# Optimization experiments

Measured on AMD Instinct MI355X. Metric: run time of the kernel, lower is better.

The kernel has to match this reference:

```python
import jax, jax.numpy as jnp
import numpy as np

N_NODES = 20000
N_RELS = 64
RP = 8
EMB = 64
N_CLASSES = 16
NT = 250000      # unique (subject, object) pairs
N_TRIPLES = 500000


def setup_inputs() -> dict:
    rng = np.random.default_rng(0)
    # sample candidate (s, o) pairs, dedupe (mirrors torch.unique(pairs, dim=0)),
    # keep exactly NT unique pairs
    cand = rng.integers(0, N_NODES, size=(NT + 60000, 2))
    pairs = np.unique(cand, axis=0)
    assert pairs.shape[0] >= NT
    pairs = pairs[:NT]
    # each triple maps to a unique-pair row and a relation column;
    # relation_matrix is the coalesced sparse_coo (nt, num_rels) densified
    row = rng.integers(0, NT, size=N_TRIPLES)
    rel = rng.integers(0, N_RELS, size=N_TRIPLES)
    relation_matrix = np.zeros((NT, N_RELS), dtype=np.float32)
    np.add.at(relation_matrix, (row, rel), 1.0)
    # hindices / vindices exactly as in __init__ (note the literal o*r / s*r):
    s, o = pairs[:, 0].astype(np.int64), pairs[:, 1].astype(np.int64)
    rm = np.arange(RP, dtype=np.int64)[:, None]
    hrow = np.tile(s, RP)                      # (RP*NT,) row in [0, N)
    hcol = (o[None, :] * rm).reshape(-1)       # (RP*NT,) col in [0, N*RP)
    vrow = (s[None, :] * rm).reshape(-1)       # (RP*NT,) row in [0, N*RP)
    vcol = np.tile(o, RP)                      # (RP*NT,) col in [0, N)

    key = jax.random.key(0)
    ks = jax.random.split(key, 6)

    def xavier(k, shape, fan_in, fan_out):
        gain = np.float32(np.sqrt(2.0))  # calculate_gain('relu')
        bound = gain * np.float32(np.sqrt(6.0 / (fan_in + fan_out)))
        return jax.random.uniform(k, shape, jnp.float32, -bound, bound)

    lb = np.float32(1.0 / np.sqrt(N_RELS))  # nn.Linear default init bound
    return {
        "relation_matrix": jnp.asarray(relation_matrix),
        "hrow": jnp.asarray(hrow), "hcol": jnp.asarray(hcol),
        "vrow": jnp.asarray(vrow), "vcol": jnp.asarray(vcol),
        "W_l1": jax.random.uniform(ks[0], (N_RELS, RP), jnp.float32, -lb, lb),
        "b_l1": jax.random.uniform(ks[1], (RP,), jnp.float32, -lb, lb),
        "W_l2": jax.random.uniform(ks[2], (N_RELS, RP), jnp.float32, -lb, lb),
        "b_l2": jax.random.uniform(ks[3], (RP,), jnp.float32, -lb, lb),
        "weights1": xavier(ks[4], (RP, N_NODES, EMB), N_NODES * EMB, RP * EMB),
        "weights2": xavier(ks[5], (RP, EMB, N_CLASSES), EMB * N_CLASSES, RP * N_CLASSES),
        "bias1": jnp.zeros((EMB,), jnp.float32),
        "bias2": jnp.zeros((N_CLASSES,), jnp.float32),
    }


def reference(relation_matrix, hrow, hcol, vrow, vcol,
              W_l1, b_l1, W_l2, b_l2, weights1, weights2, bias1, bias2):
    n, rp, e = N_NODES, RP, EMB
    nrp = n * rp
    # ---- hop 1: latent coefficients (to_latent1, ldepth=0 => single Linear)
    l1 = relation_matrix @ W_l1 + b_l1              # (NT, RP)
    l1 = l1.T.reshape(-1)                           # (RP*NT,) r-major, matches h/v index order
    # sum_sparse(hindices, l1, (n, n*rp), row=False): per-edge column-sum normalization
    colsum = jax.ops.segment_sum(l1, hcol, num_segments=nrp)
    l1 = l1 / colsum[hcol]
    # spmm over hindices: out[hrow] += l1 * weights1.view(n*rp, e)[hcol]
    Wflat = weights1.reshape(nrp, e)                # (N*RP, EMB)
    h = jax.ops.segment_sum(l1[:, None] * Wflat[hcol], hrow, num_segments=n)
    h = jax.nn.relu(h + bias1)                      # (N, EMB)
    # ---- hop 2
    l2 = jax.nn.softmax(relation_matrix @ W_l2 + b_l2, axis=1)  # (NT, RP)
    l2 = jax.nn.relu(l2.T.reshape(-1))              # (RP*NT,)
    # sum_sparse(vindices, l2, (n*rp, n), row=True): per-edge row-sum normalization
    rowsum = jax.ops.segment_sum(l2, vrow, num_segments=nrp)
    l2 = l2 / jnp.maximum(rowsum[vrow], 1e-6)
    # spmm over vindices: out[vrow] += l2 * h[vcol]
    h2 = jax.ops.segment_sum(l2[:, None] * h[vcol], vrow, num_segments=nrp)
    h2 = h2.reshape(rp, n, e)                       # (RP, N, EMB)
    logits = jnp.einsum('rhc,rnh->nc', weights2, h2) + bias2  # (N, C)
    return logits
```

## Files before the change

kernel.cpp:

```cpp
#include <hip/hip_runtime.h>
#include <hip/hip_fp16.h>

#define NT      250000
#define NN      20000
#define RP      8
#define EMB     64
#define NCLS    16
#define NRELS   64
#define COLB    547
#define REDB    64
#define KMAX    140000
#define RPB     79
#define HIB     977
#define MISCB   1250

__global__ __launch_bounds__(256) void k_gemv(
    const float* __restrict__ rm,
    const float* __restrict__ W1, const float* __restrict__ b1,
    const float* __restrict__ W2, const float* __restrict__ b2,
    float* __restrict__ l1, float* __restrict__ l2)
{
    __shared__ float tile[256 * 20];
    int t = threadIdx.x;
    int base = blockIdx.x * 256;
    float a1[8], a2[8];
#pragma unroll
    for (int r = 0; r < 8; ++r) { a1[r] = b1[r]; a2[r] = b2[r]; }

#pragma unroll 1
    for (int kc = 0; kc < 4; ++kc) {
        __syncthreads();
#pragma unroll
        for (int q = 0; q < 4; ++q) {
            int i = q * 256 + t;
            int pl = i >> 2, j4 = i & 3;
            int p = base + pl;
            float4 v = make_float4(0.f, 0.f, 0.f, 0.f);
            if (p < NT) v = reinterpret_cast<const float4*>(rm)[(size_t)p * 16 + kc * 4 + j4];
            *reinterpret_cast<float4*>(&tile[pl * 20 + j4 * 4]) = v;
        }
        __syncthreads();
        float xr[16];
#pragma unroll
        for (int j4 = 0; j4 < 4; ++j4) {
            float4 v = *reinterpret_cast<const float4*>(&tile[t * 20 + j4 * 4]);
            xr[j4 * 4 + 0] = v.x; xr[j4 * 4 + 1] = v.y;
            xr[j4 * 4 + 2] = v.z; xr[j4 * 4 + 3] = v.w;
        }
#pragma unroll
        for (int kk = 0; kk < 16; ++kk) {
            float x = xr[kk];
            int k = kc * 16 + kk;
#pragma unroll
            for (int r = 0; r < 8; ++r) {
                a1[r] = fmaf(x, W1[k * 8 + r], a1[r]);
                a2[r] = fmaf(x, W2[k * 8 + r], a2[r]);
            }
        }
    }
    int p = base + t;
    if (p >= NT) return;
    float mx = a2[0];
#pragma unroll
    for (int r = 1; r < 8; ++r) mx = fmaxf(mx, a2[r]);
    float sm = 0.f;
#pragma unroll
    for (int r = 0; r < 8; ++r) { a2[r] = __expf(a2[r] - mx); sm += a2[r]; }
    float inv = 1.0f / sm;
#pragma unroll
    for (int r = 0; r < 8; ++r) a2[r] *= inv;
    float4* o1 = reinterpret_cast<float4*>(l1 + (size_t)p * 8);
    float4* o2 = reinterpret_cast<float4*>(l2 + (size_t)p * 8);
    o1[0] = make_float4(a1[0], a1[1], a1[2], a1[3]);
    o1[1] = make_float4(a1[4], a1[5], a1[6], a1[7]);
    o2[0] = make_float4(a2[0], a2[1], a2[2], a2[3]);
    o2[1] = make_float4(a2[4], a2[5], a2[6], a2[7]);
}

__global__ __launch_bounds__(256) void k_init(
    const int* __restrict__ hrow, int* __restrict__ rowptr,
    const int* __restrict__ vcol, int* __restrict__ cnt)
{
    int bid = blockIdx.x;
    if (bid < RPB) {
        int i = bid * 256 + threadIdx.x;
        if (i > NN) return;
        int lo = 0, hi = NT;
        while (lo < hi) { int mid = (lo + hi) >> 1; if (hrow[mid] < i) lo = mid + 1; else hi = mid; }
        rowptr[i] = lo;
    } else {
        int p = (bid - RPB) * 256 + threadIdx.x;
        if (p < NT) atomicAdd(&cnt[vcol[p]], 1);
    }
}

__global__ __launch_bounds__(1024) void k_scan(
    const int* __restrict__ cnt, int* __restrict__ cstart, int* __restrict__ cnt2)
{
    __shared__ int part[1024];
    int t = threadIdx.x;
    int base = t * 20;
    int local[20];
    int s = 0;
#pragma unroll
    for (int i = 0; i < 20; ++i) {
        int idx = base + i;
        int c = (idx < NN) ? cnt[idx] : 0;
        local[i] = s;
        s += c;
    }
    part[t] = s;
    __syncthreads();
    for (int off = 1; off < 1024; off <<= 1) {
        int v = (t >= off) ? part[t - off] : 0;
        __syncthreads();
        part[t] += v;
        __syncthreads();
    }
    int ebase = t ? part[t - 1] : 0;
#pragma unroll
    for (int i = 0; i < 20; ++i) {
        int idx = base + i;
        if (idx < NN) { cstart[idx] = ebase + local[i]; cnt2[idx] = ebase + local[i]; }
    }
    if (t == 1023) cstart[NN] = part[1023];
}

__global__ __launch_bounds__(256) void k_pos(
    const int* __restrict__ vcol, int* __restrict__ cnt2, int* __restrict__ cscidx)
{
    int p = blockIdx.x * blockDim.x + threadIdx.x;
    if (p >= NT) return;
    int o = vcol[p];
    int slot = atomicAdd(&cnt2[o], 1);
    cscidx[slot] = p;
}

__global__ __launch_bounds__(256) void k_colsum(
    const float* __restrict__ l1, const int* __restrict__ cstart,
    const int* __restrict__ cscidx, float* __restrict__ colsum)
{
    int bid = blockIdx.x;
    if (bid < COLB) {
        int tid = bid * 256 + threadIdx.x;
        if (tid < NN * 7) {
            int o = tid / 7;
            int r = tid - o * 7 + 1;
            int qb = cstart[o], qe = cstart[o + 1];
            float s = 0.f;
            for (int q = qb; q < qe; ++q)
                s += l1[(size_t)cscidx[q] * 8 + r];
            atomicAdd(&colsum[o * r], s);
        }
    } else {
        int b2 = bid - COLB;
        float s = 0.f;
        for (int i = b2 * 256 + threadIdx.x; i < NT; i += REDB * 256) s += l1[(size_t)i * 8];
        __shared__ float red[256];
        red[threadIdx.x] = s;
        __syncthreads();
        for (int off = 128; off > 0; off >>= 1) {
            if (threadIdx.x < off) red[threadIdx.x] += red[threadIdx.x + off];
            __syncthreads();
        }
        if (threadIdx.x == 0) atomicAdd(&colsum[0], red[0]);
    }
}

__global__ __launch_bounds__(256) void k_inv(float* __restrict__ cs)
{
    int i = blockIdx.x * blockDim.x + threadIdx.x;
    if (i < RP * NN) cs[i] = 1.0f / cs[i];
}

__global__ __launch_bounds__(256) void k_contrib(
    const float* __restrict__ l1, const float* __restrict__ ics,
    const int* __restrict__ cstart, const int* __restrict__ cscidx,
    const float* __restrict__ w1, __half* __restrict__ contrib)
{
    int o = (int)((blockIdx.x * blockDim.x + threadIdx.x) >> 6);
    int lane = threadIdx.x & 63;
    if (o >= NN) return;
    int qb = cstart[o], qe = cstart[o + 1];
    if (qb == qe) return;
    float y[8];
    y[0] = w1[lane] * ics[0];
#pragma unroll
    for (int r = 1; r < 8; ++r) {
        int seg = o * r;
        y[r] = w1[(size_t)seg * EMB + lane] * ics[seg];
    }
    int q = qb;
    for (; q + 1 < qe; q += 2) {
        int p0 = cscidx[q], p1 = cscidx[q + 1];
        const float4* a4 = reinterpret_cast<const float4*>(l1 + (size_t)p0 * 8);
        const float4* b4 = reinterpret_cast<const float4*>(l1 + (size_t)p1 * 8);
        float4 A = a4[0], B = a4[1], C = b4[0], D = b4[1];
        float v0 = A.x * y[0];
        v0 = fmaf(A.y, y[1], v0); v0 = fmaf(A.z, y[2], v0); v0 = fmaf(A.w, y[3], v0);
        v0 = fmaf(B.x, y[4], v0); v0 = fmaf(B.y, y[5], v0);
        v0 = fmaf(B.z, y[6], v0); v0 = fmaf(B.w, y[7], v0);
        float v1 = C.x * y[0];
        v1 = fmaf(C.y, y[1], v1); v1 = fmaf(C.z, y[2], v1); v1 = fmaf(C.w, y[3], v1);
        v1 = fmaf(D.x, y[4], v1); v1 = fmaf(D.y, y[5], v1);
        v1 = fmaf(D.z, y[6], v1); v1 = fmaf(D.w, y[7], v1);
        contrib[(size_t)p0 * EMB + lane] = __float2half(v0);
        contrib[(size_t)p1 * EMB + lane] = __float2half(v1);
    }
    if (q < qe) {
        int p0 = cscidx[q];
        const float4* a4 = reinterpret_cast<const float4*>(l1 + (size_t)p0 * 8);
        float4 A = a4[0], B = a4[1];
        float v0 = A.x * y[0];
        v0 = fmaf(A.y, y[1], v0); v0 = fmaf(A.z, y[2], v0); v0 = fmaf(A.w, y[3], v0);
        v0 = fmaf(B.x, y[4], v0); v0 = fmaf(B.y, y[5], v0);
        v0 = fmaf(B.z, y[6], v0); v0 = fmaf(B.w, y[7], v0);
        contrib[(size_t)p0 * EMB + lane] = __float2half(v0);
    }
}

__global__ __launch_bounds__(256) void k_h(
    const __half* __restrict__ contrib, const float* __restrict__ l2,
    const int* __restrict__ rowptr, const float* __restrict__ bias1,
    __half* __restrict__ h, float* __restrict__ rowsum, float* __restrict__ rs0part)
{
    int s = (int)((blockIdx.x * blockDim.x + threadIdx.x) >> 6);
    int lane = threadIdx.x & 63;
    if (s >= NN) return;
    int pb = rowptr[s], pe = rowptr[s + 1];
    float acc = 0.f;
    for (int p = pb; p < pe; ++p)
        acc += __half2float(contrib[(size_t)p * EMB + lane]);
    h[(size_t)s * EMB + lane] = __float2half(fmaxf(acc + bias1[lane], 0.f));

    float psum = 0.f;
    for (int p0 = pb + (lane >> 3); p0 < pe; p0 += 8)
        psum += l2[(size_t)p0 * 8 + (lane & 7)];
    psum += __shfl_xor(psum, 8, 64);
    psum += __shfl_xor(psum, 16, 64);
    psum += __shfl_xor(psum, 32, 64);
    if (s == 0) {
        float tt = psum;
        tt += __shfl_xor(tt, 1, 64);
        tt += __shfl_xor(tt, 2, 64);
        tt += __shfl_xor(tt, 4, 64);
        if (lane == 0) rs0part[0] = tt;
    } else {
        if (lane == 0) rs0part[s] = psum;
        else if (lane < 8) atomicAdd(&rowsum[s * lane], psum);
    }
}

__global__ __launch_bounds__(256) void k_misc(
    float* __restrict__ rs, float* __restrict__ out, const float* __restrict__ b2,
    const float* __restrict__ rs0part)
{
    int bid = blockIdx.x;
    if (bid < MISCB) {
        int i = bid * 256 + threadIdx.x;
        if (i >= 1 && i < KMAX) rs[i] = 1.0f / fmaxf(rs[i], 1e-6f);
        if (i < NN * NCLS) out[i] = b2[i & (NCLS - 1)];
    } else {
        __shared__ float red[256];
        float sv = 0.f;
        for (int i = threadIdx.x; i < NN; i += 256) sv += rs0part[i];
        red[threadIdx.x] = sv;
        __syncthreads();
        for (int off = 128; off > 0; off >>= 1) {
            if (threadIdx.x < off) red[threadIdx.x] += red[threadIdx.x + off];
            __syncthreads();
        }
        if (threadIdx.x == 0) rs[0] = 1.0f / fmaxf(red[0], 1e-6f);
    }
}

__global__ __launch_bounds__(256) void k_l2out(
    const float* __restrict__ l2, const int* __restrict__ rowptr,
    const int* __restrict__ vcol, const __half* __restrict__ h,
    const float* __restrict__ irs, const float* __restrict__ w2,
    float* __restrict__ out, float* __restrict__ Abuf0)
{
    int s = (int)((blockIdx.x * blockDim.x + threadIdx.x) >> 6);
    int lane = threadIdx.x & 63;
    if (s >= NN) return;
    int pb = rowptr[s], pe = rowptr[s + 1];
    float sc[8];
#pragma unroll
    for (int rr = 1; rr < 8; ++rr) sc[rr] = (s > 0) ? irs[s * rr] : 0.f;
    float acc[8];
#pragma unroll
    for (int r = 0; r < 8; ++r) acc[r] = 0.f;
    int p = pb;
    for (; p + 3 < pe; p += 4) {
        int o0 = vcol[p], o1 = vcol[p + 1], o2 = vcol[p + 2], o3 = vcol[p + 3];
        float hv0 = __half2float(h[(size_t)o0 * EMB + lane]);
        float hv1 = __half2float(h[(size_t)o1 * EMB + lane]);
        float hv2 = __half2float(h[(size_t)o2 * EMB + lane]);
        float hv3 = __half2float(h[(size_t)o3 * EMB + lane]);
        const float4* q4 = reinterpret_cast<const float4*>(l2 + (size_t)p * 8);
        float4 A = q4[0], B = q4[1], C = q4[2], D = q4[3];
        float4 E = q4[4], F = q4[5], G = q4[6], H = q4[7];
        acc[0] = fmaf(A.x, hv0, fmaf(C.x, hv1, fmaf(E.x, hv2, fmaf(G.x, hv3, acc[0]))));
        acc[1] = fmaf(A.y, hv0, fmaf(C.y, hv1, fmaf(E.y, hv2, fmaf(G.y, hv3, acc[1]))));
        acc[2] = fmaf(A.z, hv0, fmaf(C.z, hv1, fmaf(E.z, hv2, fmaf(G.z, hv3, acc[2]))));
        acc[3] = fmaf(A.w, hv0, fmaf(C.w, hv1, fmaf(E.w, hv2, fmaf(G.w, hv3, acc[3]))));
        acc[4] = fmaf(B.x, hv0, fmaf(D.x, hv1, fmaf(F.x, hv2, fmaf(H.x, hv3, acc[4]))));
        acc[5] = fmaf(B.y, hv0, fmaf(D.y, hv1, fmaf(F.y, hv2, fmaf(H.y, hv3, acc[5]))));
        acc[6] = fmaf(B.z, hv0, fmaf(D.z, hv1, fmaf(F.z, hv2, fmaf(H.z, hv3, acc[6]))));
        acc[7] = fmaf(B.w, hv0, fmaf(D.w, hv1, fmaf(F.w, hv2, fmaf(H.w, hv3, acc[7]))));
    }
    for (; p < pe; ++p) {
        int o0 = vcol[p];
        float hv0 = __half2float(h[(size_t)o0 * EMB + lane]);
        const float4* q4 = reinterpret_cast<const float4*>(l2 + (size_t)p * 8);
        float4 A = q4[0], B = q4[1];
        acc[0] = fmaf(A.x, hv0, acc[0]); acc[1] = fmaf(A.y, hv0, acc[1]);
        acc[2] = fmaf(A.z, hv0, acc[2]); acc[3] = fmaf(A.w, hv0, acc[3]);
        acc[4] = fmaf(B.x, hv0, acc[4]); acc[5] = fmaf(B.y, hv0, acc[5]);
        acc[6] = fmaf(B.z, hv0, acc[6]); acc[7] = fmaf(B.w, hv0, acc[7]);
    }
    if (s == 0) {
        float a = acc[0] + acc[1] + acc[2] + acc[3] +
                  acc[4] + acc[5] + acc[6] + acc[7];
        Abuf0[lane] = a;
        return;
    }
    Abuf0[(size_t)s * EMB + lane] = acc[0];
    if (pb == pe) return;
    int hq = lane >> 4, c = lane & 15;
#pragma unroll
    for (int rr = 1; rr < 8; ++rr) {
        int k = s * rr;
        int rp = k / NN;
        int n  = k - rp * NN;
        float v = 0.f;
#pragma unroll
        for (int hh = 0; hh < 16; ++hh) {
            float av = __shfl(acc[rr], hq * 16 + hh, 64);
            v = fmaf(av, w2[((rp * EMB) + (hq * 16 + hh)) * NCLS + c], v);
        }
        v += __shfl_xor(v, 16, 64);
        v += __shfl_xor(v, 32, 64);
        if (lane < 16) atomicAdd(&out[(size_t)n * NCLS + lane], v * sc[rr]);
    }
}

__global__ __launch_bounds__(256) void k_redA(
    const float* __restrict__ Abuf0, float* __restrict__ h0row)
{
    __shared__ float red[256];
    int lane = threadIdx.x & 63, w = threadIdx.x >> 6;
    float sum = 0.f;
    for (int ss = blockIdx.x + 64 * w; ss < NN; ss += 256)
        sum += Abuf0[(size_t)ss * EMB + lane];
    red[threadIdx.x] = sum;
    __syncthreads();
    if (threadIdx.x < 64) {
        float v = red[threadIdx.x] + red[threadIdx.x + 64] +
                  red[threadIdx.x + 128] + red[threadIdx.x + 192];
        atomicAdd(&h0row[threadIdx.x], v);
    }
}

__global__ __launch_bounds__(64) void k_out0(
    const float* __restrict__ h0row, const float* __restrict__ irs0,
    const float* __restrict__ w2, float* __restrict__ out)
{
    int hq = threadIdx.x >> 4, c = threadIdx.x & 15;
    float v = 0.f;
#pragma unroll
    for (int hh = 0; hh < 16; ++hh) {
        int hd = hq * 16 + hh;
        v = fmaf(h0row[hd], w2[hd * NCLS + c], v);
    }
    v += __shfl_xor(v, 16, 64);
    v += __shfl_xor(v, 32, 64);
    if (threadIdx.x < 16) atomicAdd(&out[c], v * irs0[0]);
}

extern "C" void kernel_launch(void* const* d_in, const int* in_sizes, int n_in,
                              void* d_out, int out_size, void* d_ws, size_t ws_size,
                              hipStream_t stream)
{
    const float* rm    = (const float*)d_in[0];
    const int*   hrow  = (const int*)d_in[1];
    const int*   vcol  = (const int*)d_in[4];
    const float* W1    = (const float*)d_in[5];
    const float* b1    = (const float*)d_in[6];
    const float* W2    = (const float*)d_in[7];
    const float* b2    = (const float*)d_in[8];
    const float* w1    = (const float*)d_in[9];
    const float* w2    = (const float*)d_in[10];
    const float* bias1 = (const float*)d_in[11];
    const float* bias2 = (const float*)d_in[12];
    float* out = (float*)d_out;

    float* ws = (float*)d_ws;
    float*  l1      = ws;
    float*  l2      = ws + 2000000;
    int*    rowptr  = (int*)(ws + 4000000);
    float*  h0row   = ws + 4030000;
    float*  colsum  = ws + 4100000;
    float*  rowsum  = ws + 4260000;
    __half* h       = (__half*)(ws + 4400000);
    int*    cnt     = (int*)(ws + 5040000);
    int*    cstart  = cnt + 20000;
    int*    cnt2    = cstart + 20001;
    int*    cscidx  = cnt2 + 20000;
    __half* contrib = (__half*)(ws + 5600000);
    float*  Abuf0   = ws;
    float*  rs0part = ws + 1280000;

    hipMemsetAsync(colsum, 0, (size_t)160000 * sizeof(float), stream);
    hipMemsetAsync(rowsum, 0, (size_t)KMAX * sizeof(float), stream);
    hipMemsetAsync(h0row, 0, (size_t)64 * sizeof(float), stream);
    hipMemsetAsync(cnt, 0, (size_t)20000 * sizeof(int), stream);

    k_init   <<<RPB + HIB, 256, 0, stream>>>(hrow, rowptr, vcol, cnt);
    k_scan   <<<1, 1024, 0, stream>>>(cnt, cstart, cnt2);
    k_pos    <<<(NT + 255) / 256, 256, 0, stream>>>(vcol, cnt2, cscidx);
    k_gemv   <<<(NT + 255) / 256, 256, 0, stream>>>(rm, W1, b1, W2, b2, l1, l2);
    k_colsum <<<COLB + REDB, 256, 0, stream>>>(l1, cstart, cscidx, colsum);
    k_inv    <<<(RP * NN + 255) / 256, 256, 0, stream>>>(colsum);
    k_contrib<<<(NN * 64) / 256, 256, 0, stream>>>(l1, colsum, cstart, cscidx, w1, contrib);
    k_h      <<<(NN * 64) / 256, 256, 0, stream>>>(contrib, l2, rowptr, bias1, h, rowsum, rs0part);
    k_misc   <<<MISCB + 1, 256, 0, stream>>>(rowsum, out, bias2, rs0part);
    k_l2out  <<<(NN * 64) / 256, 256, 0, stream>>>(l2, rowptr, vcol, h, rowsum, w2, out, Abuf0);
    k_redA   <<<64, 256, 0, stream>>>(Abuf0, h0row);
    k_out0   <<<1, 64, 0, stream>>>(h0row, rowsum, w2, out);
}
```

Measured before the change: 251.3 us.

## Fuse init into gemv, parallelize colsum per wave, drop inverse and out0 kernels

The rowptr binary search and the vcol histogram become extra blocks of the gemv kernel, and the separate inverse kernel is removed by dividing by colsum directly in k_contrib. The out0 projection is folded into k_redA: each block projects its partial sum through w2 and atomically adds to out, so the h0row buffer and its memset go away. k_colsum is restructured to use one wavefront per column, with lanes split across 8 entries times 8 relations and a shuffle reduction, replacing the serial per-thread loop with uncoalesced reads. The aim is fewer launches and better memory parallelism; the cost is more atomics into out (one per block instead of one in total) and a divide in place of a multiply in k_contrib.

```diff
diff --git a/kernel.cpp b/kernel.cpp
--- a/kernel.cpp
+++ b/kernel.cpp
@@ -7,9 +7,9 @@
 #define EMB     64
 #define NCLS    16
 #define NRELS   64
-#define COLB    547
 #define REDB    64
 #define KMAX    140000
+#define GEMVB   977
 #define RPB     79
 #define HIB     977
 #define MISCB   1250
@@ -18,11 +18,28 @@
     const float* __restrict__ rm,
     const float* __restrict__ W1, const float* __restrict__ b1,
     const float* __restrict__ W2, const float* __restrict__ b2,
-    float* __restrict__ l1, float* __restrict__ l2)
+    float* __restrict__ l1, float* __restrict__ l2,
+    const int* __restrict__ hrow, int* __restrict__ rowptr,
+    const int* __restrict__ vcol, int* __restrict__ cnt)
 {
     __shared__ float tile[256 * 20];
+    int bid = blockIdx.x;
+    if (bid >= GEMVB) {
+        int b = bid - GEMVB;
+        if (b < RPB) {
+            int i = b * 256 + threadIdx.x;
+            if (i > NN) return;
+            int lo = 0, hi = NT;
+            while (lo < hi) { int mid = (lo + hi) >> 1; if (hrow[mid] < i) lo = mid + 1; else hi = mid; }
+            rowptr[i] = lo;
+        } else {
+            int p = (b - RPB) * 256 + threadIdx.x;
+            if (p < NT) atomicAdd(&cnt[vcol[p]], 1);
+        }
+        return;
+    }
     int t = threadIdx.x;
-    int base = blockIdx.x * 256;
+    int base = bid * 256;
     float a1[8], a2[8];
 #pragma unroll
     for (int r = 0; r < 8; ++r) { a1[r] = b1[r]; a2[r] = b2[r]; }
@@ -77,23 +94,6 @@
     o2[1] = make_float4(a2[4], a2[5], a2[6], a2[7]);
 }
 
-__global__ __launch_bounds__(256) void k_init(
-    const int* __restrict__ hrow, int* __restrict__ rowptr,
-    const int* __restrict__ vcol, int* __restrict__ cnt)
-{
-    int bid = blockIdx.x;
-    if (bid < RPB) {
-        int i = bid * 256 + threadIdx.x;
-        if (i > NN) return;
-        int lo = 0, hi = NT;
-        while (lo < hi) { int mid = (lo + hi) >> 1; if (hrow[mid] < i) lo = mid + 1; else hi = mid; }
-        rowptr[i] = lo;
-    } else {
-        int p = (bid - RPB) * 256 + threadIdx.x;
-        if (p < NT) atomicAdd(&cnt[vcol[p]], 1);
-    }
-}
-
 __global__ __launch_bounds__(1024) void k_scan(
     const int* __restrict__ cnt, int* __restrict__ cstart, int* __restrict__ cnt2)
 {
@@ -141,19 +141,23 @@
     const int* __restrict__ cscidx, float* __restrict__ colsum)
 {
     int bid = blockIdx.x;
-    if (bid < COLB) {
-        int tid = bid * 256 + threadIdx.x;
-        if (tid < NN * 7) {
-            int o = tid / 7;
-            int r = tid - o * 7 + 1;
-            int qb = cstart[o], qe = cstart[o + 1];
-            float s = 0.f;
-            for (int q = qb; q < qe; ++q)
-                s += l1[(size_t)cscidx[q] * 8 + r];
-            atomicAdd(&colsum[o * r], s);
-        }
+    if (bid < NN / 4) {
+        int o = bid * 4 + (threadIdx.x >> 6);
+        int lane = threadIdx.x & 63;
+        int qb = cstart[o], qe = cstart[o + 1];
+        if (qb == qe) return;
+        int j = lane >> 3, r = lane & 7;
+        float sum = 0.f;
+        for (int q0 = qb; q0 < qe; q0 += 8) {
+            int q = q0 + j;
+            if (q < qe) sum += l1[(size_t)cscidx[q] * 8 + r];
+        }
+        sum += __shfl_xor(sum, 8, 64);
+        sum += __shfl_xor(sum, 16, 64);
+        sum += __shfl_xor(sum, 32, 64);
+        if (lane >= 1 && lane < 8) atomicAdd(&colsum[o * lane], sum);
     } else {
-        int b2 = bid - COLB;
+        int b2 = bid - NN / 4;
         float s = 0.f;
         for (int i = b2 * 256 + threadIdx.x; i < NT; i += REDB * 256) s += l1[(size_t)i * 8];
         __shared__ float red[256];
@@ -167,14 +171,8 @@
     }
 }
 
-__global__ __launch_bounds__(256) void k_inv(float* __restrict__ cs)
-{
-    int i = blockIdx.x * blockDim.x + threadIdx.x;
-    if (i < RP * NN) cs[i] = 1.0f / cs[i];
-}
-
 __global__ __launch_bounds__(256) void k_contrib(
-    const float* __restrict__ l1, const float* __restrict__ ics,
+    const float* __restrict__ l1, const float* __restrict__ colsum,
     const int* __restrict__ cstart, const int* __restrict__ cscidx,
     const float* __restrict__ w1, __half* __restrict__ contrib)
 {
@@ -184,11 +182,11 @@
     int qb = cstart[o], qe = cstart[o + 1];
     if (qb == qe) return;
     float y[8];
-    y[0] = w1[lane] * ics[0];
+    y[0] = w1[lane] / colsum[0];
 #pragma unroll
     for (int r = 1; r < 8; ++r) {
         int seg = o * r;
-        y[r] = w1[(size_t)seg * EMB + lane] * ics[seg];
+        y[r] = w1[(size_t)seg * EMB + lane] / colsum[seg];
     }
     int q = qb;
     for (; q + 1 < qe; q += 2) {
@@ -346,9 +344,11 @@
 }
 
 __global__ __launch_bounds__(256) void k_redA(
-    const float* __restrict__ Abuf0, float* __restrict__ h0row)
+    const float* __restrict__ Abuf0, const float* __restrict__ irs,
+    const float* __restrict__ w2, float* __restrict__ out)
 {
     __shared__ float red[256];
+    __shared__ float part[64];
     int lane = threadIdx.x & 63, w = threadIdx.x >> 6;
     float sum = 0.f;
     for (int ss = blockIdx.x + 64 * w; ss < NN; ss += 256)
@@ -356,26 +356,22 @@
     red[threadIdx.x] = sum;
     __syncthreads();
     if (threadIdx.x < 64) {
-        float v = red[threadIdx.x] + red[threadIdx.x + 64] +
-                  red[threadIdx.x + 128] + red[threadIdx.x + 192];
-        atomicAdd(&h0row[threadIdx.x], v);
-    }
-}
-
-__global__ __launch_bounds__(64) void k_out0(
-    const float* __restrict__ h0row, const float* __restrict__ irs0,
-    const float* __restrict__ w2, float* __restrict__ out)
-{
-    int hq = threadIdx.x >> 4, c = threadIdx.x & 15;
-    float v = 0.f;
-#pragma unroll
-    for (int hh = 0; hh < 16; ++hh) {
-        int hd = hq * 16 + hh;
-        v = fmaf(h0row[hd], w2[hd * NCLS + c], v);
-    }
-    v += __shfl_xor(v, 16, 64);
-    v += __shfl_xor(v, 32, 64);
-    if (threadIdx.x < 16) atomicAdd(&out[c], v * irs0[0]);
+        part[threadIdx.x] = red[threadIdx.x] + red[threadIdx.x + 64] +
+                            red[threadIdx.x + 128] + red[threadIdx.x + 192];
+    }
+    __syncthreads();
+    if (threadIdx.x < 64) {
+        int hq = threadIdx.x >> 4, c = threadIdx.x & 15;
+        float v = 0.f;
+#pragma unroll
+        for (int hh = 0; hh < 16; ++hh) {
+            int hd = hq * 16 + hh;
+            v = fmaf(part[hd], w2[hd * NCLS + c], v);
+        }
+        v += __shfl_xor(v, 16, 64);
+        v += __shfl_xor(v, 32, 64);
+        if (threadIdx.x < 16) atomicAdd(&out[c], v * irs[0]);
+    }
 }
 
 extern "C" void kernel_launch(void* const* d_in, const int* in_sizes, int n_in,
@@ -399,7 +395,6 @@
     float*  l1      = ws;
     float*  l2      = ws + 2000000;
     int*    rowptr  = (int*)(ws + 4000000);
-    float*  h0row   = ws + 4030000;
     float*  colsum  = ws + 4100000;
     float*  rowsum  = ws + 4260000;
     __half* h       = (__half*)(ws + 4400000);
@@ -413,19 +408,16 @@
 
     hipMemsetAsync(colsum, 0, (size_t)160000 * sizeof(float), stream);
     hipMemsetAsync(rowsum, 0, (size_t)KMAX * sizeof(float), stream);
-    hipMemsetAsync(h0row, 0, (size_t)64 * sizeof(float), stream);
     hipMemsetAsync(cnt, 0, (size_t)20000 * sizeof(int), stream);
 
-    k_init   <<<RPB + HIB, 256, 0, stream>>>(hrow, rowptr, vcol, cnt);
+    k_gemv   <<<GEMVB + RPB + HIB, 256, 0, stream>>>(rm, W1, b1, W2, b2, l1, l2,
+                                                     hrow, rowptr, vcol, cnt);
     k_scan   <<<1, 1024, 0, stream>>>(cnt, cstart, cnt2);
     k_pos    <<<(NT + 255) / 256, 256, 0, stream>>>(vcol, cnt2, cscidx);
-    k_gemv   <<<(NT + 255) / 256, 256, 0, stream>>>(rm, W1, b1, W2, b2, l1, l2);
-    k_colsum <<<COLB + REDB, 256, 0, stream>>>(l1, cstart, cscidx, colsum);
-    k_inv    <<<(RP * NN + 255) / 256, 256, 0, stream>>>(colsum);
+    k_colsum <<<NN / 4 + REDB, 256, 0, stream>>>(l1, cstart, cscidx, colsum);
     k_contrib<<<(NN * 64) / 256, 256, 0, stream>>>(l1, colsum, cstart, cscidx, w1, contrib);
     k_h      <<<(NN * 64) / 256, 256, 0, stream>>>(contrib, l2, rowptr, bias1, h, rowsum, rs0part);
     k_misc   <<<MISCB + 1, 256, 0, stream>>>(rowsum, out, bias2, rs0part);
     k_l2out  <<<(NN * 64) / 256, 256, 0, stream>>>(l2, rowptr, vcol, h, rowsum, w2, out, Abuf0);
-    k_redA   <<<64, 256, 0, stream>>>(Abuf0, h0row);
-    k_out0   <<<1, 64, 0, stream>>>(h0row, rowsum, w2, out);
-}
+    k_redA   <<<64, 256, 0, stream>>>(Abuf0, rowsum, w2, out);
+}
```

New measurement: 233.5 us. 7.1% less time.
